# Performance work log

Measured on AMD Instinct MI355X. Metric: run time of the kernel, lower is better.

Reference implementation:

```python
import jax, jax.numpy as jnp
import numpy as np

N = 100000          # nodes
E = 3200000         # edges
D = 128             # embedding_dimension
DES = 768; TW = 768; NPROP = 5; CPROP = 3
H1, C1 = 4, 32      # gat1: 4 heads x 32 (concat -> 128)
NEXP, OUT = 2, 2    # MoE experts, output classes


def _gat(x, src, dst, W, att_src, att_dst, bias, heads, ch):
    # PyG GATConv (add_self_loops=True, negative_slope=0.2, concat)
    n = x.shape[0]
    xl = (x @ W).reshape(n, heads, ch)                      # [N,H,C]
    a_s = (xl * att_src).sum(-1)                            # [N,H]
    a_d = (xl * att_dst).sum(-1)                            # [N,H]
    loop = jnp.arange(n)
    s = jnp.concatenate([src, loop])                        # [E+N]
    d = jnp.concatenate([dst, loop])
    alpha = jax.nn.leaky_relu(a_s[s] + a_d[d], 0.2)         # [E+N,H]
    m = jax.ops.segment_max(alpha, d, num_segments=n)
    e = jnp.exp(alpha - m[d])
    z = jax.ops.segment_sum(e, d, num_segments=n)
    a = e / z[d]                                            # softmax over incoming edges
    out = jax.ops.segment_sum(xl[s] * a[:, :, None], d, num_segments=n)
    return out.reshape(n, heads * ch) + bias


def _forward(des, tweet, num_prop, cat_prop, edge_index, edge_type,
             Wd, bd, Wt, bt, Wn, bn, Wc, bc, Wi, bi,
             W1, a1s, a1d, b1, W2, a2s, a2d, b2,
             Wg, We1, be1, We2, be2):
    selu = jax.nn.selu
    x = jnp.concatenate([
        selu(des @ Wd + bd),
        selu(tweet @ Wt + bt),
        selu(num_prop @ Wn + bn),
        selu(cat_prop @ Wc + bc)], axis=1)                  # [N,128]
    x = selu(x @ Wi + bi)
    src, dst = edge_index[0], edge_index[1]
    x = _gat(x, src, dst, W1, a1s, a1d, b1, H1, C1)         # [N,128]
    # dropout(p=0.4) is identity in eval mode
    x = _gat(x, src, dst, W2, a2s, a2d, b2, 1, D)           # [N,128]
    # MoE: top-1 gating over 2 experts, experts are MLP(128->128->2, LeakyReLU)
    gates = jax.nn.softmax(x @ Wg)                          # [N,NEXP]
    topv, topi = jax.lax.top_k(gates, 1)
    topv = topv / topv.sum(-1, keepdims=True)               # =1 for k=1
    sg = jnp.zeros_like(gates).at[jnp.arange(x.shape[0])[:, None], topi].set(topv)
    h = jax.nn.leaky_relu(jnp.einsum('nd,edh->neh', x, We1) + be1, 0.01)
    o = jnp.einsum('neh,eho->neo', h, We2) + be2            # [N,NEXP,OUT]
    return (sg[:, :, None] * o).sum(1)                      # [N,OUT]


def setup_inputs():
    key = jax.random.key(0)
    ks = jax.random.split(key, 32)
    f = jnp.float32
    def w(k, shape, fan_in):
        return jax.random.normal(k, shape, f) * (1.0 / np.sqrt(fan_in))
    inp = {
        'des': jax.random.normal(ks[0], (N, DES), f),
        'tweet': jax.random.normal(ks[1], (N, TW), f),
        'num_prop': jax.random.normal(ks[2], (N, NPROP), f),
        'cat_prop': jax.random.normal(ks[3], (N, CPROP), f),
        'edge_index': jax.random.randint(ks[4], (2, E), 0, N),
        'edge_type': jax.random.randint(ks[5], (E,), 0, 3),
        'Wd': w(ks[6], (DES, D // 4), DES), 'bd': jnp.zeros((D // 4,), f),
        'Wt': w(ks[7], (TW, D // 4), TW), 'bt': jnp.zeros((D // 4,), f),
        'Wn': w(ks[8], (NPROP, D // 4), NPROP), 'bn': jnp.zeros((D // 4,), f),
        'Wc': w(ks[9], (CPROP, D // 4), CPROP), 'bc': jnp.zeros((D // 4,), f),
        'Wi': w(ks[10], (D, D), D), 'bi': jnp.zeros((D,), f),
        'W1': w(ks[11], (D, H1 * C1), D),
        'a1s': w(ks[12], (H1, C1), C1), 'a1d': w(ks[13], (H1, C1), C1),
        'b1': jnp.zeros((H1 * C1,), f),
        'W2': w(ks[14], (D, D), D),
        'a2s': w(ks[15], (1, D), D), 'a2d': w(ks[16], (1, D), D),
        'b2': jnp.zeros((D,), f),
        'Wg': w(ks[17], (D, NEXP), D),
        'We1': w(ks[18], (NEXP, D, D), D), 'be1': jnp.zeros((NEXP, D), f),
        'We2': w(ks[19], (NEXP, D, OUT), D), 'be2': jnp.zeros((NEXP, OUT), f),
    }
    return inp


def reference(des, tweet, num_prop, cat_prop, edge_index, edge_type,
              Wd, bd, Wt, bt, Wn, bn, Wc, bc, Wi, bi,
              W1, a1s, a1d, b1, W2, a2s, a2d, b2,
              Wg, We1, be1, We2, be2):
    return _forward(des, tweet, num_prop, cat_prop, edge_index, edge_type,
                    Wd, bd, Wt, bt, Wn, bn, Wc, bc, Wi, bi,
                    W1, a1s, a1d, b1, W2, a2s, a2d, b2,
                    Wg, We1, be1, We2, be2)
```

## Files before the change

### kernel.cpp

```cpp
#include <hip/hip_runtime.h>
#include <math.h>

#define NN 100000
#define NE 3200000
#define ENB 32
#define KT 64
#define X0S 132
#define NB_SCAN 391

__device__ __forceinline__ float selu_f(float x) {
    const float a = 1.6732632423543772f;
    const float s = 1.0507009873554805f;
    return x > 0.f ? s * x : s * a * (__expf(x) - 1.f);
}
__device__ __forceinline__ float lrelu02(float x)  { return fmaxf(x, 0.2f * x); }
__device__ __forceinline__ float lrelu001(float x) { return fmaxf(x, 0.01f * x); }

__global__ __launch_bounds__(256) void k_enc(
    const float* __restrict__ des, const float* __restrict__ tweet,
    const float* __restrict__ nprop, const float* __restrict__ cprop,
    const float* __restrict__ Wd, const float* __restrict__ bd,
    const float* __restrict__ Wt, const float* __restrict__ bt,
    const float* __restrict__ Wn, const float* __restrict__ bn,
    const float* __restrict__ Wc, const float* __restrict__ bc,
    const float* __restrict__ Wi, const float* __restrict__ bi,
    const float* __restrict__ W1, const float* __restrict__ a1s,
    const float* __restrict__ a1d,
    float* __restrict__ xl1, float* __restrict__ as1, float* __restrict__ ad1)
{
    __shared__ float R0[ENB * X0S];
    __shared__ float R1[ENB * X0S];
    const int t = threadIdx.x;
    const int gbase = blockIdx.x * ENB;

    {
        float* Ad = R0;
        float* At = R0 + ENB * KT;
        const int c  = t & 63;
        const int jg = t >> 6;
        const float* Wrow = (c < 32) ? (Wd + c) : (Wt + (c - 32));
        float acc[8];
#pragma unroll
        for (int j = 0; j < 8; ++j) acc[j] = 0.f;

        for (int kt0 = 0; kt0 < 768; kt0 += KT) {
            __syncthreads();
#pragma unroll
            for (int r = 0; r < 2; ++r) {
                const int idx = r * 256 + t;
                const int node = idx >> 4;
                const int q = idx & 15;
                const size_t g = (size_t)(gbase + node) * 768 + kt0 + q * 4;
                reinterpret_cast<float4*>(Ad)[idx] = *reinterpret_cast<const float4*>(des + g);
                reinterpret_cast<float4*>(At)[idx] = *reinterpret_cast<const float4*>(tweet + g);
            }
            __syncthreads();
            const float* Arow = (c < 32) ? Ad : At;
            for (int k4 = 0; k4 < KT; k4 += 4) {
                const float w0 = Wrow[(kt0 + k4 + 0) * 32];
                const float w1 = Wrow[(kt0 + k4 + 1) * 32];
                const float w2 = Wrow[(kt0 + k4 + 2) * 32];
                const float w3 = Wrow[(kt0 + k4 + 3) * 32];
#pragma unroll
                for (int j = 0; j < 8; ++j) {
                    const float4 av = *reinterpret_cast<const float4*>(&Arow[(jg * 8 + j) * KT + k4]);
                    acc[j] = fmaf(av.x, w0, fmaf(av.y, w1, fmaf(av.z, w2, fmaf(av.w, w3, acc[j]))));
                }
            }
        }
        __syncthreads();
        const float bv = (c < 32) ? bd[c] : bt[c - 32];
#pragma unroll
        for (int j = 0; j < 8; ++j)
            R0[(jg * 8 + j) * X0S + c] = selu_f(acc[j] + bv);
        if (c < 32) {
#pragma unroll
            for (int j = 0; j < 8; ++j) {
                const int node = gbase + jg * 8 + j;
                float v = 0.f;
                for (int k = 0; k < 5; ++k) v = fmaf(nprop[node * 5 + k], Wn[k * 32 + c], v);
                R0[(jg * 8 + j) * X0S + 64 + c] = selu_f(v + bn[c]);
            }
        } else {
            const int cc = c - 32;
#pragma unroll
            for (int j = 0; j < 8; ++j) {
                const int node = gbase + jg * 8 + j;
                float v = 0.f;
                for (int k = 0; k < 3; ++k) v = fmaf(cprop[node * 3 + k], Wc[k * 32 + cc], v);
                R0[(jg * 8 + j) * X0S + 96 + cc] = selu_f(v + bc[cc]);
            }
        }
    }
    __syncthreads();

    const int c  = t & 127;
    const int jg = t >> 7;

    {
        float acc[16];
#pragma unroll
        for (int j = 0; j < 16; ++j) acc[j] = 0.f;
        for (int k4 = 0; k4 < 128; k4 += 4) {
            const float w0 = Wi[(k4 + 0) * 128 + c];
            const float w1 = Wi[(k4 + 1) * 128 + c];
            const float w2 = Wi[(k4 + 2) * 128 + c];
            const float w3 = Wi[(k4 + 3) * 128 + c];
#pragma unroll
            for (int j = 0; j < 16; ++j) {
                const float4 xv = *reinterpret_cast<const float4*>(&R0[(jg * 16 + j) * X0S + k4]);
                acc[j] = fmaf(xv.x, w0, fmaf(xv.y, w1, fmaf(xv.z, w2, fmaf(xv.w, w3, acc[j]))));
            }
        }
        const float bv = bi[c];
#pragma unroll
        for (int j = 0; j < 16; ++j)
            R1[(jg * 16 + j) * X0S + c] = selu_f(acc[j] + bv);
    }
    __syncthreads();

    {
        float acc[16];
#pragma unroll
        for (int j = 0; j < 16; ++j) acc[j] = 0.f;
        for (int k4 = 0; k4 < 128; k4 += 4) {
            const float w0 = W1[(k4 + 0) * 128 + c];
            const float w1 = W1[(k4 + 1) * 128 + c];
            const float w2 = W1[(k4 + 2) * 128 + c];
            const float w3 = W1[(k4 + 3) * 128 + c];
#pragma unroll
            for (int j = 0; j < 16; ++j) {
                const float4 xv = *reinterpret_cast<const float4*>(&R1[(jg * 16 + j) * X0S + k4]);
                acc[j] = fmaf(xv.x, w0, fmaf(xv.y, w1, fmaf(xv.z, w2, fmaf(xv.w, w3, acc[j]))));
            }
        }
#pragma unroll
        for (int j = 0; j < 16; ++j)
            xl1[(size_t)(gbase + jg * 16 + j) * 128 + c] = acc[j];

        const float vs = a1s[c];
#pragma unroll
        for (int j = 0; j < 16; ++j) R0[(jg * 16 + j) * X0S + c] = acc[j] * vs;
        __syncthreads();
        if (t < 128) {
            const int node = t >> 2, h = t & 3;
            float4 s4 = make_float4(0.f, 0.f, 0.f, 0.f);
            for (int i = 0; i < 8; ++i) {
                const float4 v = *reinterpret_cast<const float4*>(&R0[node * X0S + h * 32 + i * 4]);
                s4.x += v.x; s4.y += v.y; s4.z += v.z; s4.w += v.w;
            }
            as1[(gbase + node) * 4 + h] = s4.x + s4.y + s4.z + s4.w;
        }
        __syncthreads();
        const float vd = a1d[c];
#pragma unroll
        for (int j = 0; j < 16; ++j) R0[(jg * 16 + j) * X0S + c] = acc[j] * vd;
        __syncthreads();
        if (t < 128) {
            const int node = t >> 2, h = t & 3;
            float4 s4 = make_float4(0.f, 0.f, 0.f, 0.f);
            for (int i = 0; i < 8; ++i) {
                const float4 v = *reinterpret_cast<const float4*>(&R0[node * X0S + h * 32 + i * 4]);
                s4.x += v.x; s4.y += v.y; s4.z += v.z; s4.w += v.w;
            }
            ad1[(gbase + node) * 4 + h] = s4.x + s4.y + s4.z + s4.w;
        }
    }
}

__global__ __launch_bounds__(256) void k_deg(const int* __restrict__ dst, int* __restrict__ deg) {
    const int e = blockIdx.x * 256 + threadIdx.x;
    if (e < NE) atomicAdd(&deg[dst[e]], 1);
}

__global__ __launch_bounds__(256) void k_scan1(const int* __restrict__ deg, int* __restrict__ bsum) {
    __shared__ int ws[4];
    const int t = threadIdx.x;
    const int i = blockIdx.x * 256 + t;
    int v = (i < NN) ? deg[i] : 0;
    for (int off = 32; off; off >>= 1) v += __shfl_down(v, off, 64);
    if ((t & 63) == 0) ws[t >> 6] = v;
    __syncthreads();
    if (t == 0) bsum[blockIdx.x] = ws[0] + ws[1] + ws[2] + ws[3];
}

__global__ __launch_bounds__(512) void k_scan2(const int* __restrict__ bsum,
                                               int* __restrict__ boff, int* __restrict__ rowptr) {
    __shared__ int ws[8];
    const int t = threadIdx.x;
    const int v = (t < NB_SCAN) ? bsum[t] : 0;
    int x = v;
    for (int off = 1; off < 64; off <<= 1) {
        const int u = __shfl_up(x, off, 64);
        if ((t & 63) >= off) x += u;
    }
    if ((t & 63) == 63) ws[t >> 6] = x;
    __syncthreads();
    if (t < 8) {
        int y = ws[t];
        for (int off = 1; off < 8; off <<= 1) {
            const int u = __shfl_up(y, off, 64);
            if (t >= off) y += u;
        }
        ws[t] = y;
    }
    __syncthreads();
    const int wb = (t >> 6) ? ws[(t >> 6) - 1] : 0;
    if (t < NB_SCAN) boff[t] = wb + x - v;
    if (t == NB_SCAN - 1) rowptr[NN] = wb + x;
}

__global__ __launch_bounds__(256) void k_scan3(const int* __restrict__ deg, const int* __restrict__ boff,
                                               int* __restrict__ rowptr, int* __restrict__ cursor) {
    __shared__ int ws[4];
    const int t = threadIdx.x;
    const int i = blockIdx.x * 256 + t;
    const int v = (i < NN) ? deg[i] : 0;
    int x = v;
    for (int off = 1; off < 64; off <<= 1) {
        const int u = __shfl_up(x, off, 64);
        if ((t & 63) >= off) x += u;
    }
    if ((t & 63) == 63) ws[t >> 6] = x;
    __syncthreads();
    const int wv = t >> 6;
    int wb = 0;
    for (int w = 0; w < 4; ++w) if (w < wv) wb += ws[w];
    const int excl = boff[blockIdx.x] + wb + x - v;
    if (i < NN) { rowptr[i] = excl; cursor[i] = excl; }
}

__global__ __launch_bounds__(256) void k_fill(const int* __restrict__ src, const int* __restrict__ dst,
                                              int* __restrict__ cursor, int* __restrict__ csr) {
    const int e = blockIdx.x * 256 + threadIdx.x;
    if (e < NE) {
        const int pos = atomicAdd(&cursor[dst[e]], 1);
        csr[pos] = src[e];
    }
}

__global__ __launch_bounds__(256) void k_gat1(
    const float* __restrict__ xl, const float* __restrict__ as_,
    const float* __restrict__ ad_, const float* __restrict__ b1,
    const int* __restrict__ rowptr, const int* __restrict__ csr,
    const float* __restrict__ W2, const float* __restrict__ a2s, const float* __restrict__ a2d,
    float* __restrict__ xl2, float* __restrict__ as2, float* __restrict__ ad2)
{
    __shared__ float xs[4][128];
    __shared__ float ps[4][128], pd[4][128];
    const int t = threadIdx.x;
    const int wv = t >> 6, lane = t & 63;
    const int d = blockIdx.x * 4 + wv;
    const int c0 = lane * 2;
    const int h = c0 >> 5;

    const float adv = ad_[d * 4 + h];
    const float a_self = lrelu02(as_[d * 4 + h] + adv);
    const int beg = rowptr[d], end = rowptr[d + 1];

    float m = a_self, z = 1.f;
    const float2 xv = *reinterpret_cast<const float2*>(xl + (size_t)d * 128 + c0);
    float acc0 = xv.x, acc1 = xv.y;
#pragma unroll 2
    for (int i = beg; i < end; ++i) {
        const int s = csr[i];
        const float a = lrelu02(as_[s * 4 + h] + adv);
        const float mn = fmaxf(m, a);
        const float sc = __expf(m - mn);
        const float e  = __expf(a - mn);
        const float2 v = *reinterpret_cast<const float2*>(xl + (size_t)s * 128 + c0);
        z    = fmaf(z, sc, e);
        acc0 = fmaf(acc0, sc, e * v.x);
        acc1 = fmaf(acc1, sc, e * v.y);
        m = mn;
    }
    const float inv = 1.f / z;
    xs[wv][c0]     = acc0 * inv + b1[c0];
    xs[wv][c0 + 1] = acc1 * inv + b1[c0 + 1];
    __syncthreads();

    const int base = blockIdx.x * 4;
    for (int p = 0; p < 2; ++p) {
        const int idx = p * 256 + t;
        const int n = idx >> 7, cc = idx & 127;
        float acc = 0.f;
        for (int k = 0; k < 128; k += 4) {
            acc = fmaf(xs[n][k + 0], W2[(k + 0) * 128 + cc], acc);
            acc = fmaf(xs[n][k + 1], W2[(k + 1) * 128 + cc], acc);
            acc = fmaf(xs[n][k + 2], W2[(k + 2) * 128 + cc], acc);
            acc = fmaf(xs[n][k + 3], W2[(k + 3) * 128 + cc], acc);
        }
        xl2[(size_t)(base + n) * 128 + cc] = acc;
        ps[n][cc] = acc * a2s[cc];
        pd[n][cc] = acc * a2d[cc];
    }
    __syncthreads();
    if (t < 8) {
        const int n = t >> 1, w = t & 1;
        const float* pp = w ? pd[n] : ps[n];
        float sum = 0.f;
        for (int j = 0; j < 128; ++j) sum += pp[j];
        if (w) ad2[base + n] = sum; else as2[base + n] = sum;
    }
}

__global__ __launch_bounds__(256) void k_gat2(
    const float* __restrict__ xl, const float* __restrict__ as_,
    const float* __restrict__ ad_, const float* __restrict__ b2,
    const int* __restrict__ rowptr, const int* __restrict__ csr,
    float* __restrict__ x3)
{
    const int t = threadIdx.x;
    const int wv = t >> 6, lane = t & 63;
    const int d = blockIdx.x * 4 + wv;
    const int c0 = lane * 2;

    const float adv = ad_[d];
    const float a_self = lrelu02(as_[d] + adv);
    const int beg = rowptr[d], end = rowptr[d + 1];

    float m = a_self, z = 1.f;
    const float2 xv = *reinterpret_cast<const float2*>(xl + (size_t)d * 128 + c0);
    float acc0 = xv.x, acc1 = xv.y;
#pragma unroll 2
    for (int i = beg; i < end; ++i) {
        const int s = csr[i];
        const float a = lrelu02(as_[s] + adv);
        const float mn = fmaxf(m, a);
        const float sc = __expf(m - mn);
        const float e  = __expf(a - mn);
        const float2 v = *reinterpret_cast<const float2*>(xl + (size_t)s * 128 + c0);
        z    = fmaf(z, sc, e);
        acc0 = fmaf(acc0, sc, e * v.x);
        acc1 = fmaf(acc1, sc, e * v.y);
        m = mn;
    }
    const float inv = 1.f / z;
    float2 o;
    o.x = acc0 * inv + b2[c0];
    o.y = acc1 * inv + b2[c0 + 1];
    *reinterpret_cast<float2*>(x3 + (size_t)d * 128 + c0) = o;
}

__global__ __launch_bounds__(256) void k_moe(
    const float* __restrict__ x, const float* __restrict__ Wg,
    const float* __restrict__ We1, const float* __restrict__ be1,
    const float* __restrict__ We2, const float* __restrict__ be2,
    float* __restrict__ out)
{
    __shared__ float xs[16][128];
    __shared__ float hs[16][128];
    __shared__ int sel[16];
    const int t = threadIdx.x;
    const int base = blockIdx.x * 16;

    for (int i = t; i < 16 * 128; i += 256) {
        const int n = i >> 7, cc = i & 127;
        xs[n][cc] = x[(size_t)(base + n) * 128 + cc];
    }
    __syncthreads();
    if (t < 16) {
        float g0 = 0.f, g1 = 0.f;
        for (int k = 0; k < 128; ++k) {
            g0 = fmaf(xs[t][k], Wg[k * 2 + 0], g0);
            g1 = fmaf(xs[t][k], Wg[k * 2 + 1], g1);
        }
        sel[t] = (g1 > g0) ? 1 : 0;
    }
    __syncthreads();

    const int half = t >> 7, cc = t & 127;
    const int n0 = half * 8;
    float acc[8];
#pragma unroll
    for (int i = 0; i < 8; ++i) acc[i] = 0.f;
    for (int k = 0; k < 128; ++k) {
        const float w0 = We1[k * 128 + cc];
        const float w1 = We1[128 * 128 + k * 128 + cc];
#pragma unroll
        for (int i = 0; i < 8; ++i) {
            const float w = sel[n0 + i] ? w1 : w0;
            acc[i] = fmaf(xs[n0 + i][k], w, acc[i]);
        }
    }
#pragma unroll
    for (int i = 0; i < 8; ++i) {
        const int e = sel[n0 + i];
        hs[n0 + i][cc] = lrelu001(acc[i] + be1[e * 128 + cc]);
    }
    __syncthreads();
    if (t < 32) {
        const int n = t >> 1, j = t & 1;
        const int e = sel[n];
        float o = 0.f;
        for (int k = 0; k < 128; ++k) o = fmaf(hs[n][k], We2[e * 256 + k * 2 + j], o);
        out[(size_t)(base + n) * 2 + j] = o + be2[e * 2 + j];
    }
}

extern "C" void kernel_launch(void* const* d_in, const int* in_sizes, int n_in,
                              void* d_out, int out_size, void* d_ws, size_t ws_size,
                              hipStream_t stream) {
    const float* des   = (const float*)d_in[0];
    const float* tweet = (const float*)d_in[1];
    const float* nprop = (const float*)d_in[2];
    const float* cprop = (const float*)d_in[3];
    const int*   eidx  = (const int*)d_in[4];
    const float* Wd = (const float*)d_in[6];  const float* bd = (const float*)d_in[7];
    const float* Wt = (const float*)d_in[8];  const float* bt = (const float*)d_in[9];
    const float* Wn = (const float*)d_in[10]; const float* bn = (const float*)d_in[11];
    const float* Wc = (const float*)d_in[12]; const float* bc = (const float*)d_in[13];
    const float* Wi = (const float*)d_in[14]; const float* bi = (const float*)d_in[15];
    const float* W1 = (const float*)d_in[16]; const float* a1s = (const float*)d_in[17];
    const float* a1d = (const float*)d_in[18]; const float* b1 = (const float*)d_in[19];
    const float* W2 = (const float*)d_in[20]; const float* a2s = (const float*)d_in[21];
    const float* a2d = (const float*)d_in[22]; const float* b2 = (const float*)d_in[23];
    const float* Wg = (const float*)d_in[24];
    const float* We1 = (const float*)d_in[25]; const float* be1 = (const float*)d_in[26];
    const float* We2 = (const float*)d_in[27]; const float* be2 = (const float*)d_in[28];
    float* out = (float*)d_out;

    const int* src = eidx;
    const int* dst = eidx + NE;

    float* bufA = (float*)d_ws;
    float* bufB = bufA + (size_t)NN * 128;
    float* as1  = bufB + (size_t)NN * 128;
    float* ad1  = as1 + (size_t)NN * 4;
    float* as2  = ad1 + (size_t)NN * 4;
    float* ad2  = as2 + NN;
    int* deg    = (int*)(ad2 + NN);
    int* rowptr = deg + NN;
    int* cursor = rowptr + NN + 1;
    int* csr    = cursor + NN;
    int* bsum   = csr + NE;
    int* boff   = bsum + NB_SCAN;

    hipMemsetAsync(deg, 0, NN * sizeof(int), stream);
    k_enc<<<NN / ENB, 256, 0, stream>>>(des, tweet, nprop, cprop, Wd, bd, Wt, bt, Wn, bn,
                                        Wc, bc, Wi, bi, W1, a1s, a1d, bufB, as1, ad1);
    k_deg<<<(NE + 255) / 256, 256, 0, stream>>>(dst, deg);
    k_scan1<<<NB_SCAN, 256, 0, stream>>>(deg, bsum);
    k_scan2<<<1, 512, 0, stream>>>(bsum, boff, rowptr);
    k_scan3<<<NB_SCAN, 256, 0, stream>>>(deg, boff, rowptr, cursor);
    k_fill<<<(NE + 255) / 256, 256, 0, stream>>>(src, dst, cursor, csr);
    k_gat1<<<NN / 4, 256, 0, stream>>>(bufB, as1, ad1, b1, rowptr, csr, W2, a2s, a2d,
                                       bufA, as2, ad2);
    k_gat2<<<NN / 4, 256, 0, stream>>>(bufA, as2, ad2, b2, rowptr, csr, bufB);
    k_moe<<<NN / 16, 256, 0, stream>>>(bufB, Wg, We1, be1, We2, be2, out);
}
```

Before: 2.173 ms.

## Software-pipeline GAT edge gathers and retile encoder GEMMs with shuffle reductions

The GAT aggregation loops in both layers now batch 8 edges at a time and double-buffer the CSR index loads and the feature gathers, so several gathers are in flight before the online-softmax update consumes them. The encoder kernel is retiled so each thread computes two output columns, and the shared-memory padding changes. The attention-coefficient reductions now use warp shuffles instead of extra shared-memory passes and syncs. The W2 projection in gat1 is also reorganized. The cost is higher register pressure from the buffered arrays, which could lower occupancy.

```diff
diff --git a/kernel.cpp b/kernel.cpp
--- a/kernel.cpp
+++ b/kernel.cpp
@@ -5,8 +5,10 @@
 #define NE 3200000
 #define ENB 32
 #define KT 64
-#define X0S 132
+#define SROW 68
+#define X0S 136
 #define NB_SCAN 391
+#define GP 8
 
 __device__ __forceinline__ float selu_f(float x) {
     const float a = 1.6732632423543772f;
@@ -34,136 +36,161 @@
     const int gbase = blockIdx.x * ENB;
 
     {
-        float* Ad = R0;
-        float* At = R0 + ENB * KT;
-        const int c  = t & 63;
-        const int jg = t >> 6;
-        const float* Wrow = (c < 32) ? (Wd + c) : (Wt + (c - 32));
-        float acc[8];
-#pragma unroll
-        for (int j = 0; j < 8; ++j) acc[j] = 0.f;
+        const int jg  = t >> 5;
+        const int mm  = t & 31;
+        const int mat = mm >> 4;
+        const int ch  = mm & 15;
+        const float* __restrict__ Wp = (mat ? Wt : Wd) + ch;
+        const int srow = mat * 32 + jg * 4;
+
+        float acc[2][4];
+#pragma unroll
+        for (int j = 0; j < 4; ++j) { acc[0][j] = 0.f; acc[1][j] = 0.f; }
 
         for (int kt0 = 0; kt0 < 768; kt0 += KT) {
             __syncthreads();
 #pragma unroll
-            for (int r = 0; r < 2; ++r) {
+            for (int r = 0; r < 4; ++r) {
                 const int idx = r * 256 + t;
-                const int node = idx >> 4;
+                const int row = idx >> 4;
                 const int q = idx & 15;
-                const size_t g = (size_t)(gbase + node) * 768 + kt0 + q * 4;
-                reinterpret_cast<float4*>(Ad)[idx] = *reinterpret_cast<const float4*>(des + g);
-                reinterpret_cast<float4*>(At)[idx] = *reinterpret_cast<const float4*>(tweet + g);
+                const float* bp = (row < 32) ? des : tweet;
+                const int nrow = (row < 32) ? row : row - 32;
+                const float4 v = *reinterpret_cast<const float4*>(
+                    bp + (size_t)(gbase + nrow) * 768 + kt0 + q * 4);
+                *reinterpret_cast<float4*>(&R0[row * SROW + q * 4]) = v;
             }
             __syncthreads();
-            const float* Arow = (c < 32) ? Ad : At;
             for (int k4 = 0; k4 < KT; k4 += 4) {
-                const float w0 = Wrow[(kt0 + k4 + 0) * 32];
-                const float w1 = Wrow[(kt0 + k4 + 1) * 32];
-                const float w2 = Wrow[(kt0 + k4 + 2) * 32];
-                const float w3 = Wrow[(kt0 + k4 + 3) * 32];
-#pragma unroll
-                for (int j = 0; j < 8; ++j) {
-                    const float4 av = *reinterpret_cast<const float4*>(&Arow[(jg * 8 + j) * KT + k4]);
-                    acc[j] = fmaf(av.x, w0, fmaf(av.y, w1, fmaf(av.z, w2, fmaf(av.w, w3, acc[j]))));
+                const float wl0 = Wp[(kt0 + k4 + 0) * 32];
+                const float wl1 = Wp[(kt0 + k4 + 1) * 32];
+                const float wl2 = Wp[(kt0 + k4 + 2) * 32];
+                const float wl3 = Wp[(kt0 + k4 + 3) * 32];
+                const float wh0 = Wp[(kt0 + k4 + 0) * 32 + 16];
+                const float wh1 = Wp[(kt0 + k4 + 1) * 32 + 16];
+                const float wh2 = Wp[(kt0 + k4 + 2) * 32 + 16];
+                const float wh3 = Wp[(kt0 + k4 + 3) * 32 + 16];
+#pragma unroll
+                for (int j = 0; j < 4; ++j) {
+                    const float4 av = *reinterpret_cast<const float4*>(&R0[(srow + j) * SROW + k4]);
+                    acc[0][j] = fmaf(av.x, wl0, fmaf(av.y, wl1, fmaf(av.z, wl2, fmaf(av.w, wl3, acc[0][j]))));
+                    acc[1][j] = fmaf(av.x, wh0, fmaf(av.y, wh1, fmaf(av.z, wh2, fmaf(av.w, wh3, acc[1][j]))));
                 }
             }
         }
         __syncthreads();
-        const float bv = (c < 32) ? bd[c] : bt[c - 32];
-#pragma unroll
-        for (int j = 0; j < 8; ++j)
-            R0[(jg * 8 + j) * X0S + c] = selu_f(acc[j] + bv);
-        if (c < 32) {
+        const float blo = mat ? bt[ch] : bd[ch];
+        const float bhi = mat ? bt[ch + 16] : bd[ch + 16];
+#pragma unroll
+        for (int j = 0; j < 4; ++j) {
+            const int node = jg * 4 + j;
+            R0[node * X0S + mat * 32 + ch]      = selu_f(acc[0][j] + blo);
+            R0[node * X0S + mat * 32 + ch + 16] = selu_f(acc[1][j] + bhi);
+        }
+        const int ch64 = t & 63;
+        const int ng = t >> 6;
+        if (ch64 < 32) {
+            const float bv = bn[ch64];
 #pragma unroll
             for (int j = 0; j < 8; ++j) {
-                const int node = gbase + jg * 8 + j;
+                const int node = ng * 8 + j;
+                const float* r = nprop + (size_t)(gbase + node) * 5;
                 float v = 0.f;
-                for (int k = 0; k < 5; ++k) v = fmaf(nprop[node * 5 + k], Wn[k * 32 + c], v);
-                R0[(jg * 8 + j) * X0S + 64 + c] = selu_f(v + bn[c]);
+                for (int k = 0; k < 5; ++k) v = fmaf(r[k], Wn[k * 32 + ch64], v);
+                R0[node * X0S + 64 + ch64] = selu_f(v + bv);
             }
         } else {
-            const int cc = c - 32;
+            const int cc = ch64 - 32;
+            const float bv = bc[cc];
 #pragma unroll
             for (int j = 0; j < 8; ++j) {
-                const int node = gbase + jg * 8 + j;
+                const int node = ng * 8 + j;
+                const float* r = cprop + (size_t)(gbase + node) * 3;
                 float v = 0.f;
-                for (int k = 0; k < 3; ++k) v = fmaf(cprop[node * 3 + k], Wc[k * 32 + cc], v);
-                R0[(jg * 8 + j) * X0S + 96 + cc] = selu_f(v + bc[cc]);
-            }
-        }
-    }
-    __syncthreads();
-
-    const int c  = t & 127;
-    const int jg = t >> 7;
+                for (int k = 0; k < 3; ++k) v = fmaf(r[k], Wc[k * 32 + cc], v);
+                R0[node * X0S + 96 + cc] = selu_f(v + bv);
+            }
+        }
+    }
+    __syncthreads();
+
+    const int c  = t & 63;
+    const int g2 = t >> 6;
 
     {
-        float acc[16];
-#pragma unroll
-        for (int j = 0; j < 16; ++j) acc[j] = 0.f;
+        float acc[2][8];
+#pragma unroll
+        for (int j = 0; j < 8; ++j) { acc[0][j] = 0.f; acc[1][j] = 0.f; }
         for (int k4 = 0; k4 < 128; k4 += 4) {
-            const float w0 = Wi[(k4 + 0) * 128 + c];
-            const float w1 = Wi[(k4 + 1) * 128 + c];
-            const float w2 = Wi[(k4 + 2) * 128 + c];
-            const float w3 = Wi[(k4 + 3) * 128 + c];
-#pragma unroll
-            for (int j = 0; j < 16; ++j) {
-                const float4 xv = *reinterpret_cast<const float4*>(&R0[(jg * 16 + j) * X0S + k4]);
-                acc[j] = fmaf(xv.x, w0, fmaf(xv.y, w1, fmaf(xv.z, w2, fmaf(xv.w, w3, acc[j]))));
-            }
-        }
-        const float bv = bi[c];
-#pragma unroll
-        for (int j = 0; j < 16; ++j)
-            R1[(jg * 16 + j) * X0S + c] = selu_f(acc[j] + bv);
+            const float wl0 = Wi[(k4 + 0) * 128 + c];
+            const float wl1 = Wi[(k4 + 1) * 128 + c];
+            const float wl2 = Wi[(k4 + 2) * 128 + c];
+            const float wl3 = Wi[(k4 + 3) * 128 + c];
+            const float wh0 = Wi[(k4 + 0) * 128 + c + 64];
+            const float wh1 = Wi[(k4 + 1) * 128 + c + 64];
+            const float wh2 = Wi[(k4 + 2) * 128 + c + 64];
+            const float wh3 = Wi[(k4 + 3) * 128 + c + 64];
+#pragma unroll
+            for (int j = 0; j < 8; ++j) {
+                const float4 xv = *reinterpret_cast<const float4*>(&R0[(g2 * 8 + j) * X0S + k4]);
+                acc[0][j] = fmaf(xv.x, wl0, fmaf(xv.y, wl1, fmaf(xv.z, wl2, fmaf(xv.w, wl3, acc[0][j]))));
+                acc[1][j] = fmaf(xv.x, wh0, fmaf(xv.y, wh1, fmaf(xv.z, wh2, fmaf(xv.w, wh3, acc[1][j]))));
+            }
+        }
+        const float blo = bi[c], bhi = bi[c + 64];
+#pragma unroll
+        for (int j = 0; j < 8; ++j) {
+            R1[(g2 * 8 + j) * X0S + c]      = selu_f(acc[0][j] + blo);
+            R1[(g2 * 8 + j) * X0S + c + 64] = selu_f(acc[1][j] + bhi);
+        }
     }
     __syncthreads();
 
     {
-        float acc[16];
-#pragma unroll
-        for (int j = 0; j < 16; ++j) acc[j] = 0.f;
+        float acc[2][8];
+#pragma unroll
+        for (int j = 0; j < 8; ++j) { acc[0][j] = 0.f; acc[1][j] = 0.f; }
         for (int k4 = 0; k4 < 128; k4 += 4) {
-            const float w0 = W1[(k4 + 0) * 128 + c];
-            const float w1 = W1[(k4 + 1) * 128 + c];
-            const float w2 = W1[(k4 + 2) * 128 + c];
-            const float w3 = W1[(k4 + 3) * 128 + c];
-#pragma unroll
-            for (int j = 0; j < 16; ++j) {
-                const float4 xv = *reinterpret_cast<const float4*>(&R1[(jg * 16 + j) * X0S + k4]);
-                acc[j] = fmaf(xv.x, w0, fmaf(xv.y, w1, fmaf(xv.z, w2, fmaf(xv.w, w3, acc[j]))));
-            }
-        }
-#pragma unroll
-        for (int j = 0; j < 16; ++j)
-            xl1[(size_t)(gbase + jg * 16 + j) * 128 + c] = acc[j];
-
-        const float vs = a1s[c];
-#pragma unroll
-        for (int j = 0; j < 16; ++j) R0[(jg * 16 + j) * X0S + c] = acc[j] * vs;
-        __syncthreads();
-        if (t < 128) {
-            const int node = t >> 2, h = t & 3;
-            float4 s4 = make_float4(0.f, 0.f, 0.f, 0.f);
-            for (int i = 0; i < 8; ++i) {
-                const float4 v = *reinterpret_cast<const float4*>(&R0[node * X0S + h * 32 + i * 4]);
-                s4.x += v.x; s4.y += v.y; s4.z += v.z; s4.w += v.w;
-            }
-            as1[(gbase + node) * 4 + h] = s4.x + s4.y + s4.z + s4.w;
-        }
-        __syncthreads();
-        const float vd = a1d[c];
-#pragma unroll
-        for (int j = 0; j < 16; ++j) R0[(jg * 16 + j) * X0S + c] = acc[j] * vd;
-        __syncthreads();
-        if (t < 128) {
-            const int node = t >> 2, h = t & 3;
-            float4 s4 = make_float4(0.f, 0.f, 0.f, 0.f);
-            for (int i = 0; i < 8; ++i) {
-                const float4 v = *reinterpret_cast<const float4*>(&R0[node * X0S + h * 32 + i * 4]);
-                s4.x += v.x; s4.y += v.y; s4.z += v.z; s4.w += v.w;
-            }
-            ad1[(gbase + node) * 4 + h] = s4.x + s4.y + s4.z + s4.w;
+            const float wl0 = W1[(k4 + 0) * 128 + c];
+            const float wl1 = W1[(k4 + 1) * 128 + c];
+            const float wl2 = W1[(k4 + 2) * 128 + c];
+            const float wl3 = W1[(k4 + 3) * 128 + c];
+            const float wh0 = W1[(k4 + 0) * 128 + c + 64];
+            const float wh1 = W1[(k4 + 1) * 128 + c + 64];
+            const float wh2 = W1[(k4 + 2) * 128 + c + 64];
+            const float wh3 = W1[(k4 + 3) * 128 + c + 64];
+#pragma unroll
+            for (int j = 0; j < 8; ++j) {
+                const float4 xv = *reinterpret_cast<const float4*>(&R1[(g2 * 8 + j) * X0S + k4]);
+                acc[0][j] = fmaf(xv.x, wl0, fmaf(xv.y, wl1, fmaf(xv.z, wl2, fmaf(xv.w, wl3, acc[0][j]))));
+                acc[1][j] = fmaf(xv.x, wh0, fmaf(xv.y, wh1, fmaf(xv.z, wh2, fmaf(xv.w, wh3, acc[1][j]))));
+            }
+        }
+        const float slo = a1s[c], shi = a1s[c + 64];
+        const float dlo = a1d[c], dhi = a1d[c + 64];
+#pragma unroll
+        for (int j = 0; j < 8; ++j) {
+            const size_t node = (size_t)gbase + g2 * 8 + j;
+            xl1[node * 128 + c]      = acc[0][j];
+            xl1[node * 128 + c + 64] = acc[1][j];
+            float v0 = acc[0][j] * slo;
+            float v1 = acc[1][j] * shi;
+            float v2 = acc[0][j] * dlo;
+            float v3 = acc[1][j] * dhi;
+#pragma unroll
+            for (int off = 16; off; off >>= 1) {
+                v0 += __shfl_xor(v0, off, 32);
+                v1 += __shfl_xor(v1, off, 32);
+                v2 += __shfl_xor(v2, off, 32);
+                v3 += __shfl_xor(v3, off, 32);
+            }
+            if ((c & 31) == 0) {
+                const int hh = c >> 5;
+                as1[node * 4 + hh]     = v0;
+                as1[node * 4 + 2 + hh] = v1;
+                ad1[node * 4 + hh]     = v2;
+                ad1[node * 4 + 2 + hh] = v3;
+            }
         }
     }
 }
@@ -254,53 +281,103 @@
     const int c0 = lane * 2;
     const int h = c0 >> 5;
 
-    const float adv = ad_[d * 4 + h];
-    const float a_self = lrelu02(as_[d * 4 + h] + adv);
+    const float adv = ad_[(size_t)d * 4 + h];
+    const float a_self = lrelu02(as_[(size_t)d * 4 + h] + adv);
     const int beg = rowptr[d], end = rowptr[d + 1];
+    const int nb = (end - beg + GP - 1) / GP;
 
     float m = a_self, z = 1.f;
     const float2 xv = *reinterpret_cast<const float2*>(xl + (size_t)d * 128 + c0);
     float acc0 = xv.x, acc1 = xv.y;
-#pragma unroll 2
-    for (int i = beg; i < end; ++i) {
-        const int s = csr[i];
-        const float a = lrelu02(as_[s * 4 + h] + adv);
-        const float mn = fmaxf(m, a);
-        const float sc = __expf(m - mn);
-        const float e  = __expf(a - mn);
-        const float2 v = *reinterpret_cast<const float2*>(xl + (size_t)s * 128 + c0);
-        z    = fmaf(z, sc, e);
-        acc0 = fmaf(acc0, sc, e * v.x);
-        acc1 = fmaf(acc1, sc, e * v.y);
-        m = mn;
+
+    int sA[GP], sB[GP];
+    float aA[GP], aB[GP];
+    float2 vA[GP], vB[GP];
+
+    auto CSRL = [&](int b, int (&sb)[GP]) {
+#pragma unroll
+        for (int j = 0; j < GP; ++j) {
+            const int idx = beg + b * GP + j;
+            sb[j] = (idx < end) ? csr[idx] : -1;
+        }
+    };
+    auto GATH = [&](const int (&sb)[GP], float (&ab)[GP], float2 (&vb)[GP]) {
+#pragma unroll
+        for (int j = 0; j < GP; ++j) {
+            const int s = sb[j];
+            const int sa = (s < 0) ? d : s;
+            const float av = as_[(size_t)sa * 4 + h];
+            ab[j] = (s < 0) ? -INFINITY : av;
+            vb[j] = *reinterpret_cast<const float2*>(xl + (size_t)sa * 128 + c0);
+        }
+    };
+    auto PROC = [&](const float (&ab)[GP], const float2 (&vb)[GP]) {
+#pragma unroll
+        for (int j = 0; j < GP; ++j) {
+            const float a = lrelu02(ab[j] + adv);
+            const float mn = fmaxf(m, a);
+            const float sc = __expf(m - mn);
+            const float e  = __expf(a - mn);
+            z    = fmaf(z, sc, e);
+            acc0 = fmaf(acc0, sc, e * vb[j].x);
+            acc1 = fmaf(acc1, sc, e * vb[j].y);
+            m = mn;
+        }
+    };
+
+    if (nb > 0) {
+        CSRL(0, sA);
+        if (nb > 1) CSRL(1, sB);
+        GATH(sA, aA, vA);
+        int b = 0;
+        while (true) {
+            if (b + 1 < nb) GATH(sB, aB, vB);
+            if (b + 2 < nb) CSRL(b + 2, sA);
+            PROC(aA, vA);
+            if (++b >= nb) break;
+            if (b + 1 < nb) GATH(sA, aA, vA);
+            if (b + 2 < nb) CSRL(b + 2, sB);
+            PROC(aB, vB);
+            if (++b >= nb) break;
+        }
     }
     const float inv = 1.f / z;
-    xs[wv][c0]     = acc0 * inv + b1[c0];
-    xs[wv][c0 + 1] = acc1 * inv + b1[c0 + 1];
+    xs[wv][c0]     = fmaf(acc0, inv, b1[c0]);
+    xs[wv][c0 + 1] = fmaf(acc1, inv, b1[c0 + 1]);
     __syncthreads();
 
     const int base = blockIdx.x * 4;
-    for (int p = 0; p < 2; ++p) {
-        const int idx = p * 256 + t;
-        const int n = idx >> 7, cc = idx & 127;
-        float acc = 0.f;
-        for (int k = 0; k < 128; k += 4) {
-            acc = fmaf(xs[n][k + 0], W2[(k + 0) * 128 + cc], acc);
-            acc = fmaf(xs[n][k + 1], W2[(k + 1) * 128 + cc], acc);
-            acc = fmaf(xs[n][k + 2], W2[(k + 2) * 128 + cc], acc);
-            acc = fmaf(xs[n][k + 3], W2[(k + 3) * 128 + cc], acc);
-        }
-        xl2[(size_t)(base + n) * 128 + cc] = acc;
-        ps[n][cc] = acc * a2s[cc];
-        pd[n][cc] = acc * a2d[cc];
-    }
-    __syncthreads();
-    if (t < 8) {
-        const int n = t >> 1, w = t & 1;
-        const float* pp = w ? pd[n] : ps[n];
-        float sum = 0.f;
-        for (int j = 0; j < 128; ++j) sum += pp[j];
-        if (w) ad2[base + n] = sum; else as2[base + n] = sum;
+    const int cc = t & 127;
+    const int np = (t >> 7) * 2;
+    {
+        float g0 = 0.f, g1 = 0.f;
+        for (int k4 = 0; k4 < 128; k4 += 4) {
+            const float w0 = W2[(k4 + 0) * 128 + cc];
+            const float w1 = W2[(k4 + 1) * 128 + cc];
+            const float w2 = W2[(k4 + 2) * 128 + cc];
+            const float w3 = W2[(k4 + 3) * 128 + cc];
+            const float4 x0v = *reinterpret_cast<const float4*>(&xs[np][k4]);
+            const float4 x1v = *reinterpret_cast<const float4*>(&xs[np + 1][k4]);
+            g0 = fmaf(x0v.x, w0, fmaf(x0v.y, w1, fmaf(x0v.z, w2, fmaf(x0v.w, w3, g0))));
+            g1 = fmaf(x1v.x, w0, fmaf(x1v.y, w1, fmaf(x1v.z, w2, fmaf(x1v.w, w3, g1))));
+        }
+        xl2[(size_t)(base + np) * 128 + cc]     = g0;
+        xl2[(size_t)(base + np + 1) * 128 + cc] = g1;
+        const float s2 = a2s[cc], d2 = a2d[cc];
+        ps[np][cc] = g0 * s2;     pd[np][cc] = g0 * d2;
+        ps[np + 1][cc] = g1 * s2; pd[np + 1][cc] = g1 * d2;
+    }
+    __syncthreads();
+    {
+        const int tn = t & 127;
+        const int node = tn >> 5, q = tn & 31;
+        const float* pp = (t < 128) ? ps[node] : pd[node];
+        float v = pp[q] + pp[q + 32] + pp[q + 64] + pp[q + 96];
+#pragma unroll
+        for (int off = 16; off; off >>= 1) v += __shfl_xor(v, off, 32);
+        if (q == 0) {
+            if (t < 128) as2[base + node] = v; else ad2[base + node] = v;
+        }
     }
 }
 
@@ -318,27 +395,67 @@
     const float adv = ad_[d];
     const float a_self = lrelu02(as_[d] + adv);
     const int beg = rowptr[d], end = rowptr[d + 1];
+    const int nb = (end - beg + GP - 1) / GP;
 
     float m = a_self, z = 1.f;
     const float2 xv = *reinterpret_cast<const float2*>(xl + (size_t)d * 128 + c0);
     float acc0 = xv.x, acc1 = xv.y;
-#pragma unroll 2
-    for (int i = beg; i < end; ++i) {
-        const int s = csr[i];
-        const float a = lrelu02(as_[s] + adv);
-        const float mn = fmaxf(m, a);
-        const float sc = __expf(m - mn);
-        const float e  = __expf(a - mn);
-        const float2 v = *reinterpret_cast<const float2*>(xl + (size_t)s * 128 + c0);
-        z    = fmaf(z, sc, e);
-        acc0 = fmaf(acc0, sc, e * v.x);
-        acc1 = fmaf(acc1, sc, e * v.y);
-        m = mn;
+
+    int sA[GP], sB[GP];
+    float aA[GP], aB[GP];
+    float2 vA[GP], vB[GP];
+
+    auto CSRL = [&](int b, int (&sb)[GP]) {
+#pragma unroll
+        for (int j = 0; j < GP; ++j) {
+            const int idx = beg + b * GP + j;
+            sb[j] = (idx < end) ? csr[idx] : -1;
+        }
+    };
+    auto GATH = [&](const int (&sb)[GP], float (&ab)[GP], float2 (&vb)[GP]) {
+#pragma unroll
+        for (int j = 0; j < GP; ++j) {
+            const int s = sb[j];
+            const int sa = (s < 0) ? d : s;
+            const float av = as_[sa];
+            ab[j] = (s < 0) ? -INFINITY : av;
+            vb[j] = *reinterpret_cast<const float2*>(xl + (size_t)sa * 128 + c0);
+        }
+    };
+    auto PROC = [&](const float (&ab)[GP], const float2 (&vb)[GP]) {
+#pragma unroll
+        for (int j = 0; j < GP; ++j) {
+            const float a = lrelu02(ab[j] + adv);
+            const float mn = fmaxf(m, a);
+            const float sc = __expf(m - mn);
+            const float e  = __expf(a - mn);
+            z    = fmaf(z, sc, e);
+            acc0 = fmaf(acc0, sc, e * vb[j].x);
+            acc1 = fmaf(acc1, sc, e * vb[j].y);
+            m = mn;
+        }
+    };
+
+    if (nb > 0) {
+        CSRL(0, sA);
+        if (nb > 1) CSRL(1, sB);
+        GATH(sA, aA, vA);
+        int b = 0;
+        while (true) {
+            if (b + 1 < nb) GATH(sB, aB, vB);
+            if (b + 2 < nb) CSRL(b + 2, sA);
+            PROC(aA, vA);
+            if (++b >= nb) break;
+            if (b + 1 < nb) GATH(sA, aA, vA);
+            if (b + 2 < nb) CSRL(b + 2, sB);
+            PROC(aB, vB);
+            if (++b >= nb) break;
+        }
     }
     const float inv = 1.f / z;
     float2 o;
-    o.x = acc0 * inv + b2[c0];
-    o.y = acc1 * inv + b2[c0 + 1];
+    o.x = fmaf(acc0, inv, b2[c0]);
+    o.y = fmaf(acc1, inv, b2[c0 + 1]);
     *reinterpret_cast<float2*>(x3 + (size_t)d * 128 + c0) = o;
 }
 
```

Measured after the change: 2.034 ms. 1.07x faster.
